# Performance work log

Measured on AMD Instinct MI355X. Metric: run time of the kernel, lower is better.

The kernel has to match this reference:

```python
import jax, jax.numpy as jnp
import numpy as np

B, NFIELD, NEMB, NFILTER, NLAYERS = 256, 64, 64, 128, 3


def setup_inputs() -> dict:
    key = jax.random.key(0)
    ks = jax.random.split(key, 5)
    x = jax.random.normal(ks[0], (B, NFIELD, NEMB), dtype=jnp.float32)
    # Conv1d(k=1, bias=False) weights, squeezed to (out_ch, in_ch). Small init for stability.
    W0 = jax.random.normal(ks[1], (NFILTER, NFIELD * NFIELD), dtype=jnp.float32) * 0.02
    W1 = jax.random.normal(ks[2], (NFILTER, NFIELD * NFILTER), dtype=jnp.float32) * 0.02
    W2 = jax.random.normal(ks[3], (NFILTER, NFIELD * NFILTER), dtype=jnp.float32) * 0.02
    Wa = jax.random.normal(ks[4], (1, NLAYERS * NFILTER), dtype=jnp.float32) * 0.02
    return {"x": x, "W0": W0, "W1": W1, "W2": W2, "Wa": Wa}


def reference(x, W0, W1, W2, Wa):
    # x: (B, F, E). CIN recurrence over a fixed small number of layers.
    Ws = [W0, W1, W2]
    x0 = x
    xk = x
    pooled = []
    for W in Ws:
        # outer product over field axes: (B, F, C, E)
        h = x0[:, :, None, :] * xk[:, None, :, :]
        b, f, c, e = h.shape
        h = h.reshape(b, f * c, e)
        # 1x1 conv == GEMM over channel dim, then ReLU
        xk = jax.nn.relu(jnp.einsum('oc,bce->boe', W, h))
        # sum-pool over embedding dim: (B, nfilter)
        pooled.append(jnp.sum(xk, axis=-1))
    feats = jnp.concatenate(pooled, axis=1)  # (B, nlayers*nfilter)
    y = feats @ Wa.T                         # (B, 1)
    return y[:, 0]
```

## Files before the change

### kernel.cpp

```cpp
#include <hip/hip_runtime.h>

#define NBATCH 256
#define NFILT  128

typedef __attribute__((ext_vector_type(8))) short bf16x8;
typedef __attribute__((ext_vector_type(4))) float f32x4;

__device__ __forceinline__ unsigned short f2b(float f) {
    unsigned u = __float_as_uint(f);
    u = (u + 0x7fffu + ((u >> 16) & 1u)) >> 16;
    return (unsigned short)u;
}
__device__ __forceinline__ float b2f(unsigned short h) {
    return __uint_as_float(((unsigned)h) << 16);
}
__device__ __forceinline__ void async16(const void* g, void* l) {
    __builtin_amdgcn_global_load_lds((const __attribute__((address_space(1))) unsigned int*)g,
                                     (__attribute__((address_space(3))) unsigned int*)l, 16, 0, 0);
}

#define XKA_OFF 0
#define XKB_OFF 16384
#define X0T_OFF 32768
#define RED_OFF 40960
#define YS_OFF  139264
#define SMEM_SZ 139328

__global__ void prep_w(const float* __restrict__ W, unsigned short* __restrict__ Wp,
                       int CLOG, int KLOG) {
    int idx = blockIdx.x * 256 + threadIdx.x;
    int o = idx >> KLOG;
    int k = idx & ((1 << KLOG) - 1);
    int f = k >> CLOG, c = k & ((1 << CLOG) - 1);
    int kg = f >> 4, fl = f & 15;
    int cs = c >> 5, kseg = (c >> 3) & 3, j = c & 7;
    int mh = o >> 6, mt = (o >> 4) & 3, l15 = o & 15;
    int ncs = 1 << (CLOG - 5);
    size_t dst = ((((size_t)((kg * 16 + fl) * ncs + cs) * 2 + mh) * 4 + mt) * 64
                  + kseg * 16 + l15) * 8 + j;
    Wp[dst] = f2b(W[idx]);
}

__global__ void prep_x(const float* __restrict__ x, unsigned short* __restrict__ x0t) {
    int idx = blockIdx.x * 256 + threadIdx.x;
    int b = idx >> 12, r = idx & 4095, f = r >> 6, e = r & 63;
    x0t[b * 4096 + e * 64 + ((((f >> 3) ^ (e & 7)) << 3) | (f & 7))] = f2b(x[idx]);
}

template<int NCS, int ROWB, bool LAST>
__device__ __forceinline__ void do_layer(
    const char* __restrict__ Ag,
    const char* __restrict__ XKsrc,
    char* __restrict__ XKdst,
    const char* __restrict__ X0T,
    char* __restrict__ RED,
    const float* __restrict__ Wa_l,
    float& ypart, int lane, int l15, int kseg, int e7, int mh, int kg)
{
    const f32x4 ZERO = {0.f, 0.f, 0.f, 0.f};
    f32x4 acc[4][4];
#pragma unroll
    for (int mt = 0; mt < 4; ++mt)
#pragma unroll
        for (int nt = 0; nt < 4; ++nt) acc[mt][nt] = ZERO;
    f32x4 accf[4][4];
    bf16x8 a0[4], a1[4], b0[4], b1[4];
    const char* bbase[4];
#pragma unroll
    for (int nt = 0; nt < 4; ++nt) bbase[nt] = XKsrc + (nt * 16 + l15) * ROWB;

#define LD_A(ks, A) { _Pragma("unroll") for (int mt_ = 0; mt_ < 4; ++mt_) \
    A[mt_] = *(const bf16x8*)(Ag + (ks) * 8192 + mt_ * 1024); }
#define LD_B(ks, Bv) { const int csn_ = (ks) & (NCS - 1); \
    _Pragma("unroll") for (int nt_ = 0; nt_ < 4; ++nt_) \
    Bv[nt_] = *(const bf16x8*)(bbase[nt_] + ((((csn_ << 2) + kseg) ^ e7) << 4)); }
#define MM(A, Bv, FIRST) { _Pragma("unroll") for (int mt_ = 0; mt_ < 4; ++mt_) \
    _Pragma("unroll") for (int nt_ = 0; nt_ < 4; ++nt_) \
    accf[mt_][nt_] = __builtin_amdgcn_mfma_f32_16x16x32_bf16(A[mt_], Bv[nt_], \
        (FIRST) ? ZERO : accf[mt_][nt_], 0, 0, 0); }

    LD_A(0, a0); LD_B(0, b0);
    for (int fl = 0; fl < 16; ++fl) {
        const int fg = kg * 16 + fl;
        const int fsw = (((fg >> 3) ^ e7) << 4) | ((fg & 7) << 1);
        float x0v[4];
#pragma unroll
        for (int nt = 0; nt < 4; ++nt)
            x0v[nt] = b2f(*(const unsigned short*)(X0T + (nt * 16 + l15) * 128 + fsw));
        const int ks0 = fl * NCS;
#pragma unroll
        for (int cs = 0; cs < NCS; ++cs) {
            const int nks = ks0 + cs + 1;
            if (cs & 1) {
                if (cs < NCS - 1)      { LD_A(nks, a0); LD_B(nks, b0); }
                else if (fl < 15)      { LD_A(nks, a0); LD_B(nks, b0); }
                MM(a1, b1, cs == 0);
            } else {
                if (cs < NCS - 1)      { LD_A(nks, a1); LD_B(nks, b1); }
                else if (fl < 15)      { LD_A(nks, a1); LD_B(nks, b1); }
                MM(a0, b0, cs == 0);
            }
        }
#pragma unroll
        for (int nt = 0; nt < 4; ++nt) {
            const f32x4 xv = {x0v[nt], x0v[nt], x0v[nt], x0v[nt]};
#pragma unroll
            for (int mt = 0; mt < 4; ++mt)
                acc[mt][nt] += accf[mt][nt] * xv;
        }
    }
#undef LD_A
#undef LD_B
#undef MM

    if (kg != 0) {
        char* slot = RED + (mh * 3 + (kg - 1)) * 16384;
#pragma unroll
        for (int mt = 0; mt < 4; ++mt)
#pragma unroll
            for (int nt = 0; nt < 4; ++nt)
                *(f32x4*)(slot + ((mt * 4 + nt) * 64 + lane) * 16) = acc[mt][nt];
    }
    __syncthreads();
    if (kg == 0) {
#pragma unroll
        for (int s = 0; s < 3; ++s) {
            const char* slot = RED + (mh * 3 + s) * 16384;
#pragma unroll
            for (int mt = 0; mt < 4; ++mt)
#pragma unroll
                for (int nt = 0; nt < 4; ++nt)
                    acc[mt][nt] += *(const f32x4*)(slot + ((mt * 4 + nt) * 64 + lane) * 16);
        }
        const int r0 = (lane >> 4) * 4;
#pragma unroll
        for (int mt = 0; mt < 4; ++mt) {
            const int om = mh * 64 + mt * 16 + r0;
            const float4 wa = *(const float4*)(Wa_l + om);
            const int osw = (((om >> 3) ^ e7) << 4) | ((om & 7) << 1);
#pragma unroll
            for (int nt = 0; nt < 4; ++nt) {
                f32x4 v = acc[mt][nt];
                v.x = fmaxf(v.x, 0.f); v.y = fmaxf(v.y, 0.f);
                v.z = fmaxf(v.z, 0.f); v.w = fmaxf(v.w, 0.f);
                ypart = fmaf(wa.x, v.x, ypart);
                ypart = fmaf(wa.y, v.y, ypart);
                ypart = fmaf(wa.z, v.z, ypart);
                ypart = fmaf(wa.w, v.w, ypart);
                if (!LAST) {
                    unsigned lo = (unsigned)f2b(v.x) | ((unsigned)f2b(v.y) << 16);
                    unsigned hi = (unsigned)f2b(v.z) | ((unsigned)f2b(v.w) << 16);
                    *(uint2*)(XKdst + (nt * 16 + l15) * 256 + osw) = make_uint2(lo, hi);
                }
            }
        }
    }
    __syncthreads();
}

__global__ __launch_bounds__(512, 2) void cin_main(
    const unsigned short* __restrict__ Wp0,
    const unsigned short* __restrict__ Wp1,
    const unsigned short* __restrict__ Wp2,
    const unsigned short* __restrict__ x0t,
    const float* __restrict__ Wa,
    float* __restrict__ y)
{
    extern __shared__ char sm[];
    const int b = blockIdx.x, tid = threadIdx.x;
    const int lane = tid & 63, w = tid >> 6;
    const int mh = w & 1, kg = w >> 1;
    const int l15 = lane & 15, kseg = lane >> 4, e7 = lane & 7;

    async16((const char*)x0t + (size_t)b * 8192 + w * 1024 + lane * 16,
            sm + X0T_OFF + w * 1024);
    __syncthreads();

    float ypart = 0.f;
    const char* Ag0 = (const char*)Wp0 + (size_t)kg * 16 * 2 * 8192 + mh * 4096 + lane * 16;
    do_layer<2, 128, false>(Ag0, sm + X0T_OFF, sm + XKA_OFF, sm + X0T_OFF, sm + RED_OFF,
                            Wa + 0, ypart, lane, l15, kseg, e7, mh, kg);
    const char* Ag1 = (const char*)Wp1 + (size_t)kg * 16 * 4 * 8192 + mh * 4096 + lane * 16;
    do_layer<4, 256, false>(Ag1, sm + XKA_OFF, sm + XKB_OFF, sm + X0T_OFF, sm + RED_OFF,
                            Wa + 128, ypart, lane, l15, kseg, e7, mh, kg);
    const char* Ag2 = (const char*)Wp2 + (size_t)kg * 16 * 4 * 8192 + mh * 4096 + lane * 16;
    do_layer<4, 256, true>(Ag2, sm + XKB_OFF, sm + XKA_OFF, sm + X0T_OFF, sm + RED_OFF,
                           Wa + 256, ypart, lane, l15, kseg, e7, mh, kg);

#pragma unroll
    for (int off = 32; off >= 1; off >>= 1)
        ypart += __shfl_down(ypart, off, 64);
    float* YS = (float*)(sm + YS_OFF);
    if (lane == 0 && kg == 0) YS[mh] = ypart;
    __syncthreads();
    if (tid == 0) y[b] = YS[0] + YS[1];
}

extern "C" void kernel_launch(void* const* d_in, const int* in_sizes, int n_in,
                              void* d_out, int out_size, void* d_ws, size_t ws_size,
                              hipStream_t stream) {
    const float* x  = (const float*)d_in[0];
    const float* W0 = (const float*)d_in[1];
    const float* W1 = (const float*)d_in[2];
    const float* W2 = (const float*)d_in[3];
    const float* Wa = (const float*)d_in[4];
    float* y = (float*)d_out;

    char* ws = (char*)d_ws;
    unsigned short* Wp0 = (unsigned short*)(ws);
    unsigned short* Wp1 = (unsigned short*)(ws + (1u << 20));
    unsigned short* Wp2 = (unsigned short*)(ws + (3u << 20));
    unsigned short* x0t = (unsigned short*)(ws + (5u << 20));

    hipLaunchKernelGGL(prep_w, dim3(2048), dim3(256), 0, stream, W0, Wp0, 6, 12);
    hipLaunchKernelGGL(prep_w, dim3(4096), dim3(256), 0, stream, W1, Wp1, 7, 13);
    hipLaunchKernelGGL(prep_w, dim3(4096), dim3(256), 0, stream, W2, Wp2, 7, 13);
    hipLaunchKernelGGL(prep_x, dim3(4096), dim3(256), 0, stream, x, x0t);

    hipFuncSetAttribute((const void*)cin_main, hipFuncAttributeMaxDynamicSharedMemorySize, SMEM_SZ);
    hipLaunchKernelGGL(cin_main, dim3(NBATCH), dim3(512), SMEM_SZ, stream,
                       Wp0, Wp1, Wp2, x0t, Wa, y);
}
```

Measured before the change: 106.9 us.

## Merge prep kernels, hoist per-layer B fragments into registers, add field-major x0 copy

The four preprocessing launches become one combined kernel, which also writes a second, field-major bf16 copy of x0. In the main kernel, all B fragments for a layer are loaded from LDS into registers once, since they do not depend on the field index, rather than being reloaded for every field. The x0 scalars are then read as contiguous values from the new field-major LDS buffer, and A loads are double-buffered a single step ahead. This cuts LDS traffic and launch overhead, at the cost of more registers for B fragments (risking spills at 512 threads with 2 blocks per CU) and extra shared memory.

```diff
diff --git a/kernel.cpp b/kernel.cpp
--- a/kernel.cpp
+++ b/kernel.cpp
@@ -22,29 +22,43 @@
 #define XKA_OFF 0
 #define XKB_OFF 16384
 #define X0T_OFF 32768
-#define RED_OFF 40960
-#define YS_OFF  139264
-#define SMEM_SZ 139328
-
-__global__ void prep_w(const float* __restrict__ W, unsigned short* __restrict__ Wp,
-                       int CLOG, int KLOG) {
-    int idx = blockIdx.x * 256 + threadIdx.x;
-    int o = idx >> KLOG;
-    int k = idx & ((1 << KLOG) - 1);
-    int f = k >> CLOG, c = k & ((1 << CLOG) - 1);
-    int kg = f >> 4, fl = f & 15;
-    int cs = c >> 5, kseg = (c >> 3) & 3, j = c & 7;
-    int mh = o >> 6, mt = (o >> 4) & 3, l15 = o & 15;
-    int ncs = 1 << (CLOG - 5);
-    size_t dst = ((((size_t)((kg * 16 + fl) * ncs + cs) * 2 + mh) * 4 + mt) * 64
-                  + kseg * 16 + l15) * 8 + j;
-    Wp[dst] = f2b(W[idx]);
-}
-
-__global__ void prep_x(const float* __restrict__ x, unsigned short* __restrict__ x0t) {
-    int idx = blockIdx.x * 256 + threadIdx.x;
-    int b = idx >> 12, r = idx & 4095, f = r >> 6, e = r & 63;
-    x0t[b * 4096 + e * 64 + ((((f >> 3) ^ (e & 7)) << 3) | (f & 7))] = f2b(x[idx]);
+#define X0F_OFF 40960
+#define RED_OFF 49152
+#define YS_OFF  147456
+#define SMEM_SZ 147520
+
+__global__ void prep_all(const float* __restrict__ x,
+                         const float* __restrict__ W0,
+                         const float* __restrict__ W1,
+                         const float* __restrict__ W2,
+                         unsigned short* __restrict__ x0t,
+                         unsigned short* __restrict__ x0f,
+                         unsigned short* __restrict__ Wp0,
+                         unsigned short* __restrict__ Wp1,
+                         unsigned short* __restrict__ Wp2)
+{
+    const int bid = blockIdx.x, tid = threadIdx.x;
+    if (bid < 10240) {
+        const float* W; unsigned short* Wp; int CLOG, KLOG, idx;
+        if (bid < 2048)      { W = W0; Wp = Wp0; CLOG = 6; KLOG = 12; idx = bid * 256 + tid; }
+        else if (bid < 6144) { W = W1; Wp = Wp1; CLOG = 7; KLOG = 13; idx = (bid - 2048) * 256 + tid; }
+        else                 { W = W2; Wp = Wp2; CLOG = 7; KLOG = 13; idx = (bid - 6144) * 256 + tid; }
+        int o = idx >> KLOG, k = idx & ((1 << KLOG) - 1);
+        int f = k >> CLOG, c = k & ((1 << CLOG) - 1);
+        int kg = f >> 4, fl = f & 15;
+        int cs = c >> 5, kseg = (c >> 3) & 3, j = c & 7;
+        int mh = o >> 6, mt = (o >> 4) & 3, l15 = o & 15;
+        int ncs = 1 << (CLOG - 5);
+        size_t dst = ((((size_t)((kg * 16 + fl) * ncs + cs) * 2 + mh) * 4 + mt) * 64
+                      + kseg * 16 + l15) * 8 + j;
+        Wp[dst] = f2b(W[idx]);
+    } else {
+        int idx = (bid - 10240) * 256 + tid;
+        int b = idx >> 12, r = idx & 4095, f = r >> 6, e = r & 63;
+        unsigned short v = f2b(x[idx]);
+        x0f[b * 4096 + f * 64 + e] = v;
+        x0t[b * 4096 + e * 64 + ((((f >> 3) ^ (e & 7)) << 3) | (f & 7))] = v;
+    }
 }
 
 template<int NCS, int ROWB, bool LAST>
@@ -52,7 +66,7 @@
     const char* __restrict__ Ag,
     const char* __restrict__ XKsrc,
     char* __restrict__ XKdst,
-    const char* __restrict__ X0T,
+    const char* __restrict__ X0F,
     char* __restrict__ RED,
     const float* __restrict__ Wa_l,
     float& ypart, int lane, int l15, int kseg, int e7, int mh, int kg)
@@ -63,55 +77,50 @@
     for (int mt = 0; mt < 4; ++mt)
 #pragma unroll
         for (int nt = 0; nt < 4; ++nt) acc[mt][nt] = ZERO;
+
+    bf16x8 bq[NCS][4];
+#pragma unroll
+    for (int cs = 0; cs < NCS; ++cs)
+#pragma unroll
+        for (int nt = 0; nt < 4; ++nt)
+            bq[cs][nt] = *(const bf16x8*)(XKsrc + (nt * 16 + l15) * ROWB
+                                          + ((((cs << 2) + kseg) ^ e7) << 4));
+
+    bf16x8 aq[2][4];
+#pragma unroll
+    for (int mt = 0; mt < 4; ++mt)
+        aq[0][mt] = *(const bf16x8*)(Ag + mt * 1024);
+
     f32x4 accf[4][4];
-    bf16x8 a0[4], a1[4], b0[4], b1[4];
-    const char* bbase[4];
-#pragma unroll
-    for (int nt = 0; nt < 4; ++nt) bbase[nt] = XKsrc + (nt * 16 + l15) * ROWB;
-
-#define LD_A(ks, A) { _Pragma("unroll") for (int mt_ = 0; mt_ < 4; ++mt_) \
-    A[mt_] = *(const bf16x8*)(Ag + (ks) * 8192 + mt_ * 1024); }
-#define LD_B(ks, Bv) { const int csn_ = (ks) & (NCS - 1); \
-    _Pragma("unroll") for (int nt_ = 0; nt_ < 4; ++nt_) \
-    Bv[nt_] = *(const bf16x8*)(bbase[nt_] + ((((csn_ << 2) + kseg) ^ e7) << 4)); }
-#define MM(A, Bv, FIRST) { _Pragma("unroll") for (int mt_ = 0; mt_ < 4; ++mt_) \
-    _Pragma("unroll") for (int nt_ = 0; nt_ < 4; ++nt_) \
-    accf[mt_][nt_] = __builtin_amdgcn_mfma_f32_16x16x32_bf16(A[mt_], Bv[nt_], \
-        (FIRST) ? ZERO : accf[mt_][nt_], 0, 0, 0); }
-
-    LD_A(0, a0); LD_B(0, b0);
     for (int fl = 0; fl < 16; ++fl) {
-        const int fg = kg * 16 + fl;
-        const int fsw = (((fg >> 3) ^ e7) << 4) | ((fg & 7) << 1);
-        float x0v[4];
-#pragma unroll
-        for (int nt = 0; nt < 4; ++nt)
-            x0v[nt] = b2f(*(const unsigned short*)(X0T + (nt * 16 + l15) * 128 + fsw));
-        const int ks0 = fl * NCS;
+        const unsigned short* xf = (const unsigned short*)(X0F + ((kg * 16 + fl) << 7));
+        const float x0v0 = b2f(xf[l15]);
+        const float x0v1 = b2f(xf[16 + l15]);
+        const float x0v2 = b2f(xf[32 + l15]);
+        const float x0v3 = b2f(xf[48 + l15]);
+        const size_t ksf = (size_t)fl * NCS;
 #pragma unroll
         for (int cs = 0; cs < NCS; ++cs) {
-            const int nks = ks0 + cs + 1;
-            if (cs & 1) {
-                if (cs < NCS - 1)      { LD_A(nks, a0); LD_B(nks, b0); }
-                else if (fl < 15)      { LD_A(nks, a0); LD_B(nks, b0); }
-                MM(a1, b1, cs == 0);
-            } else {
-                if (cs < NCS - 1)      { LD_A(nks, a1); LD_B(nks, b1); }
-                else if (fl < 15)      { LD_A(nks, a1); LD_B(nks, b1); }
-                MM(a0, b0, cs == 0);
-            }
-        }
-#pragma unroll
-        for (int nt = 0; nt < 4; ++nt) {
-            const f32x4 xv = {x0v[nt], x0v[nt], x0v[nt], x0v[nt]};
 #pragma unroll
             for (int mt = 0; mt < 4; ++mt)
-                acc[mt][nt] += accf[mt][nt] * xv;
-        }
-    }
-#undef LD_A
-#undef LD_B
-#undef MM
+                aq[(cs + 1) & 1][mt] =
+                    *(const bf16x8*)(Ag + (ksf + cs + 1) * 8192 + mt * 1024);
+#pragma unroll
+            for (int mt = 0; mt < 4; ++mt)
+#pragma unroll
+                for (int nt = 0; nt < 4; ++nt)
+                    accf[mt][nt] = __builtin_amdgcn_mfma_f32_16x16x32_bf16(
+                        aq[cs & 1][mt], bq[cs][nt],
+                        (cs == 0) ? ZERO : accf[mt][nt], 0, 0, 0);
+        }
+#pragma unroll
+        for (int mt = 0; mt < 4; ++mt) {
+            acc[mt][0] += accf[mt][0] * x0v0;
+            acc[mt][1] += accf[mt][1] * x0v1;
+            acc[mt][2] += accf[mt][2] * x0v2;
+            acc[mt][3] += accf[mt][3] * x0v3;
+        }
+    }
 
     if (kg != 0) {
         char* slot = RED + (mh * 3 + (kg - 1)) * 16384;
@@ -163,6 +172,7 @@
     const unsigned short* __restrict__ Wp1,
     const unsigned short* __restrict__ Wp2,
     const unsigned short* __restrict__ x0t,
+    const unsigned short* __restrict__ x0f,
     const float* __restrict__ Wa,
     float* __restrict__ y)
 {
@@ -174,17 +184,19 @@
 
     async16((const char*)x0t + (size_t)b * 8192 + w * 1024 + lane * 16,
             sm + X0T_OFF + w * 1024);
+    async16((const char*)x0f + (size_t)b * 8192 + w * 1024 + lane * 16,
+            sm + X0F_OFF + w * 1024);
     __syncthreads();
 
     float ypart = 0.f;
     const char* Ag0 = (const char*)Wp0 + (size_t)kg * 16 * 2 * 8192 + mh * 4096 + lane * 16;
-    do_layer<2, 128, false>(Ag0, sm + X0T_OFF, sm + XKA_OFF, sm + X0T_OFF, sm + RED_OFF,
+    do_layer<2, 128, false>(Ag0, sm + X0T_OFF, sm + XKA_OFF, sm + X0F_OFF, sm + RED_OFF,
                             Wa + 0, ypart, lane, l15, kseg, e7, mh, kg);
     const char* Ag1 = (const char*)Wp1 + (size_t)kg * 16 * 4 * 8192 + mh * 4096 + lane * 16;
-    do_layer<4, 256, false>(Ag1, sm + XKA_OFF, sm + XKB_OFF, sm + X0T_OFF, sm + RED_OFF,
+    do_layer<4, 256, false>(Ag1, sm + XKA_OFF, sm + XKB_OFF, sm + X0F_OFF, sm + RED_OFF,
                             Wa + 128, ypart, lane, l15, kseg, e7, mh, kg);
     const char* Ag2 = (const char*)Wp2 + (size_t)kg * 16 * 4 * 8192 + mh * 4096 + lane * 16;
-    do_layer<4, 256, true>(Ag2, sm + XKB_OFF, sm + XKA_OFF, sm + X0T_OFF, sm + RED_OFF,
+    do_layer<4, 256, true>(Ag2, sm + XKB_OFF, sm + XKA_OFF, sm + X0F_OFF, sm + RED_OFF,
                            Wa + 256, ypart, lane, l15, kseg, e7, mh, kg);
 
 #pragma unroll
@@ -211,13 +223,12 @@
     unsigned short* Wp1 = (unsigned short*)(ws + (1u << 20));
     unsigned short* Wp2 = (unsigned short*)(ws + (3u << 20));
     unsigned short* x0t = (unsigned short*)(ws + (5u << 20));
-
-    hipLaunchKernelGGL(prep_w, dim3(2048), dim3(256), 0, stream, W0, Wp0, 6, 12);
-    hipLaunchKernelGGL(prep_w, dim3(4096), dim3(256), 0, stream, W1, Wp1, 7, 13);
-    hipLaunchKernelGGL(prep_w, dim3(4096), dim3(256), 0, stream, W2, Wp2, 7, 13);
-    hipLaunchKernelGGL(prep_x, dim3(4096), dim3(256), 0, stream, x, x0t);
+    unsigned short* x0f = (unsigned short*)(ws + (7u << 20));
+
+    hipLaunchKernelGGL(prep_all, dim3(14336), dim3(256), 0, stream,
+                       x, W0, W1, W2, x0t, x0f, Wp0, Wp1, Wp2);
 
     hipFuncSetAttribute((const void*)cin_main, hipFuncAttributeMaxDynamicSharedMemorySize, SMEM_SZ);
     hipLaunchKernelGGL(cin_main, dim3(NBATCH), dim3(512), SMEM_SZ, stream,
-                       Wp0, Wp1, Wp2, x0t, Wa, y);
-}
+                       Wp0, Wp1, Wp2, x0t, x0f, Wa, y);
+}
```

After: 102.2 us. 1.05x faster.
